# Performance work log

Measured on AMD Instinct MI355X. Metric: run time of the kernel, lower is better.

The kernel has to match this reference:

```python
import jax, jax.numpy as jnp
import numpy as np

B, T, H, POOL, MAX_ITER = 32, 1024, 128, 16, 4
D = 2 * H  # feature size of U rows


def _maxout(x, w, b, out_dim, pool):
    # x: [..., fin], w: [fin, out_dim*pool], b: [out_dim*pool]
    y = x @ w + b
    y = y.reshape(y.shape[:-1] + (out_dim, pool))
    return y.max(axis=-1)


def _hmn(U, us, ue, h, WDw, WDb, W1w, W1b, W2w, W2b, W3w, W3b):
    # U: [B,T,2H]; us, ue: [B,2H]; h: [B,H] -> scores [B,T]
    r = jnp.tanh(jnp.concatenate([h, us, ue], axis=-1) @ WDw + WDb)  # [B,H]
    rt = jnp.broadcast_to(r[:, None, :], (U.shape[0], U.shape[1], r.shape[-1]))
    m1 = _maxout(jnp.concatenate([U, rt], axis=-1), W1w, W1b, H, POOL)  # [B,T,H]
    m2 = _maxout(m1, W2w, W2b, H, POOL)                                  # [B,T,H]
    m3 = _maxout(jnp.concatenate([m1, m2], axis=-1), W3w, W3b, 1, POOL)  # [B,T,1]
    return m3[..., 0]  # [B,T]


def _lstm_cell(x, h, c, wih, whh, bih, bhh):
    gates = x @ wih.T + bih + h @ whh.T + bhh  # [B,4H]
    i, f, g, o = jnp.split(gates, 4, axis=-1)
    i, f, o = jax.nn.sigmoid(i), jax.nn.sigmoid(f), jax.nn.sigmoid(o)
    g = jnp.tanh(g)
    c2 = f * c + i * g
    h2 = o * jnp.tanh(c2)
    return h2, c2


def setup_inputs() -> dict:
    key = jax.random.key(0)
    ks = jax.random.split(key, 24)
    s = 0.05
    gn = lambda k, shape: (jax.random.normal(k, shape, jnp.float32) * s)
    inp = {"U": jax.random.normal(ks[0], (B, T, D), jnp.float32)}
    for tag, off in (("s", 1), ("e", 9)):
        inp[f"WD{tag}_w"] = gn(ks[off + 0], (5 * H, H))
        inp[f"WD{tag}_b"] = jnp.zeros((H,), jnp.float32)
        inp[f"W1{tag}_w"] = gn(ks[off + 1], (3 * H, H * POOL))
        inp[f"W1{tag}_b"] = jnp.zeros((H * POOL,), jnp.float32)
        inp[f"W2{tag}_w"] = gn(ks[off + 2], (H, H * POOL))
        inp[f"W2{tag}_b"] = jnp.zeros((H * POOL,), jnp.float32)
        inp[f"W3{tag}_w"] = gn(ks[off + 3], (2 * H, POOL))
        inp[f"W3{tag}_b"] = jnp.zeros((POOL,), jnp.float32)
    inp["lstm_wih"] = gn(ks[20], (4 * H, 4 * H))
    inp["lstm_whh"] = gn(ks[21], (4 * H, H))
    inp["lstm_bih"] = jnp.zeros((4 * H,), jnp.float32)
    inp["lstm_bhh"] = jnp.zeros((4 * H,), jnp.float32)
    return inp


def reference(U,
              WDs_w, WDs_b, W1s_w, W1s_b, W2s_w, W2s_b, W3s_w, W3s_b,
              WDe_w, WDe_b, W1e_w, W1e_b, W2e_w, W2e_b, W3e_w, W3e_b,
              lstm_wih, lstm_whh, lstm_bih, lstm_bhh):
    b = U.shape[0]
    bidx = jnp.arange(b)
    h = jnp.zeros((b, H), U.dtype)
    c = jnp.zeros((b, H), U.dtype)
    us, ue = U[:, 0, :], U[:, 1, :]
    entropies = []
    for _ in range(MAX_ITER):  # training-mode: run all iterations (no host-sync early stop)
        alpha_sc = _hmn(U, us, ue, h, WDs_w, WDs_b, W1s_w, W1s_b, W2s_w, W2s_b, W3s_w, W3s_b)
        alpha = jnp.argmax(alpha_sc, axis=1)           # [B]
        us = U[bidx, alpha, :]                          # data-dependent gather
        beta_sc = _hmn(U, us, ue, h, WDe_w, WDe_b, W1e_w, W1e_b, W2e_w, W2e_b, W3e_w, W3e_b)
        beta = jnp.argmax(beta_sc, axis=1)
        ue = U[bidx, beta, :]
        h, c = _lstm_cell(jnp.concatenate([us, ue], axis=1), h, c,
                          lstm_wih, lstm_whh, lstm_bih, lstm_bhh)
        entropies.append(jnp.stack([alpha_sc, beta_sc], axis=0))
    ent = jnp.stack(entropies, axis=0)  # [max_iter, 2, B, T]
    return alpha, beta, ent
```

## Files before the change

kernel.cpp:

```cpp
#include <hip/hip_runtime.h>
#include <math.h>

static constexpr int cB = 32;
static constexpr int cT = 1024;
static constexpr int cH = 128;
static constexpr int cD = 256;
static constexpr int cN = 2048;
static constexpr int cM = cB * cT;

typedef __attribute__((ext_vector_type(8))) short short8;
typedef __attribute__((ext_vector_type(4))) float f32x4;

__device__ __forceinline__ ushort f2bf(float x) {
    union { float f; unsigned u; } v; v.f = x;
    unsigned r = v.u + 0x7FFF + ((v.u >> 16) & 1);
    return (ushort)(r >> 16);
}
__device__ __forceinline__ float bf2f(ushort h) {
    union { float f; unsigned u; } v; v.u = ((unsigned)h) << 16;
    return v.f;
}

__device__ __forceinline__ void gload_lds16(const ushort* g, ushort* l) {
    __builtin_amdgcn_global_load_lds(
        (const __attribute__((address_space(1))) unsigned int*)(const void*)g,
        (__attribute__((address_space(3))) unsigned int*)(void*)l,
        16, 0, 0);
}

__global__ __launch_bounds__(256, 2)
void mfma_pool_m2(const ushort* __restrict__ Wth, const ushort* __restrict__ Wtl,
                  const ushort* __restrict__ Xh, const ushort* __restrict__ Xl,
                  const float* __restrict__ bias, float* __restrict__ out)
{
    constexpr int K = 128, S = 4;
    __shared__ __attribute__((aligned(16))) ushort sWh[128 * 128];
    __shared__ __attribute__((aligned(16))) ushort sWl[128 * 128];

    const int tid  = threadIdx.x;
    const int wave = tid >> 6;
    const int lane = tid & 63;
    const int l15  = lane & 15;
    const int lg   = lane >> 4;
    const int wr   = wave >> 1;
    const int wc   = wave & 1;

    const int wg  = blockIdx.x;
    const int lin = (wg & 7) * 128 + (wg >> 3);
    const int bx  = lin & 15;
    const int by  = lin >> 4;
    const int n0  = bx * 128;

    float ivv[4][4];
    #pragma unroll
    for (int rf = 0; rf < 4; ++rf)
        #pragma unroll
        for (int r = 0; r < 4; ++r)
            ivv[rf][r] = bias[n0 + wr * 64 + rf * 16 + lg * 4 + r];

    const int st_row_lo = lane >> 4;
    const int st_slot   = lane & 15;
    #pragma unroll
    for (int j = 0; j < 8; ++j) {
        int i   = wave * 8 + j;
        int row = i * 4 + st_row_lo;
        int ck  = st_slot ^ (row & 7);
        size_t goff = (size_t)(n0 + row) * K + ck * 8;
        gload_lds16(Wth + goff, sWh + i * 512);
        gload_lds16(Wtl + goff, sWl + i * 512);
    }
    __syncthreads();

    const int NP = 128;
    #pragma unroll
    for (int s = 0; s < S; ++s) {
        const int m0 = by * 512 + s * 128;

        short8 xh_[16], xl_[16];
        #pragma unroll
        for (int cf = 0; cf < 4; ++cf)
            #pragma unroll
            for (int ks = 0; ks < 4; ++ks) {
                size_t off = (size_t)(m0 + wc * 64 + cf * 16 + l15) * K
                           + ks * 32 + lg * 8;
                xh_[cf * 4 + ks] = *(const short8*)(Xh + off);
                xl_[cf * 4 + ks] = *(const short8*)(Xl + off);
            }

        f32x4 acc[4][4];
        #pragma unroll
        for (int rf = 0; rf < 4; ++rf)
            #pragma unroll
            for (int cf = 0; cf < 4; ++cf)
                acc[rf][cf] = (f32x4){0.f, 0.f, 0.f, 0.f};

        #pragma unroll
        for (int ks = 0; ks < 4; ++ks) {
            short8 w_h[4], w_l[4];
            #pragma unroll
            for (int rf = 0; rf < 4; ++rf) {
                int row  = wr * 64 + rf * 16 + l15;
                int ck2  = ks * 4 + lg;
                int adr  = row * 128 + ((ck2 ^ (row & 7)) * 8);
                w_h[rf] = *(const short8*)(sWh + adr);
                w_l[rf] = *(const short8*)(sWl + adr);
            }
            #pragma unroll
            for (int rf = 0; rf < 4; ++rf)
                #pragma unroll
                for (int cf = 0; cf < 4; ++cf) {
                    acc[rf][cf] = __builtin_amdgcn_mfma_f32_16x16x32_bf16(
                        w_h[rf], xh_[cf * 4 + ks], acc[rf][cf], 0, 0, 0);
                    acc[rf][cf] = __builtin_amdgcn_mfma_f32_16x16x32_bf16(
                        w_l[rf], xh_[cf * 4 + ks], acc[rf][cf], 0, 0, 0);
                    acc[rf][cf] = __builtin_amdgcn_mfma_f32_16x16x32_bf16(
                        w_h[rf], xl_[cf * 4 + ks], acc[rf][cf], 0, 0, 0);
                }
        }

        #pragma unroll
        for (int rf = 0; rf < 4; ++rf) {
            const int o2 = (n0 >> 4) + wr * 4 + rf;
            #pragma unroll
            for (int cf = 0; cf < 4; ++cf) {
                float v0 = acc[rf][cf][0] + ivv[rf][0];
                float v1 = acc[rf][cf][1] + ivv[rf][1];
                float v2 = acc[rf][cf][2] + ivv[rf][2];
                float v3 = acc[rf][cf][3] + ivv[rf][3];
                float mx = fmaxf(fmaxf(v0, v1), fmaxf(v2, v3));
                mx = fmaxf(mx, __shfl_xor(mx, 16));
                mx = fmaxf(mx, __shfl_xor(mx, 32));
                if (lane < 16) {
                    int m = m0 + wc * 64 + cf * 16 + lane;
                    out[(size_t)m * NP + o2] = mx;
                }
            }
        }
    }
}

template<int K, bool WRITE_HL>
__global__ __launch_bounds__(256, 2)
void mfma_pool_swp(const ushort* __restrict__ Wth, const ushort* __restrict__ Wtl,
                   const ushort* __restrict__ Xh, const ushort* __restrict__ Xl,
                   const float* __restrict__ initv, int init_bstride,
                   float* __restrict__ out, ushort* __restrict__ outh,
                   ushort* __restrict__ outl)
{
    constexpr int KH = K / 128;
    __shared__ __attribute__((aligned(16))) ushort sWh[128 * 128];
    __shared__ __attribute__((aligned(16))) ushort sWl[128 * 128];

    const int tid  = threadIdx.x;
    const int wave = tid >> 6;
    const int lane = tid & 63;
    const int l15  = lane & 15;
    const int lg   = lane >> 4;
    const int wr   = wave >> 1;
    const int wc   = wave & 1;

    const int wg  = blockIdx.x;
    const int lin = (wg & 7) * 512 + (wg >> 3);
    const int bx  = lin & 15;
    const int by  = lin >> 4;
    const int n0  = bx * 128;
    const int m0  = by * 128;
    const size_t ibase = (size_t)(m0 >> 10) * init_bstride;

    float ivv[4][4];
    #pragma unroll
    for (int rf = 0; rf < 4; ++rf)
        #pragma unroll
        for (int r = 0; r < 4; ++r)
            ivv[rf][r] = initv[ibase + n0 + wr * 64 + rf * 16 + lg * 4 + r];

    f32x4 acc[4][4];
    #pragma unroll
    for (int rf = 0; rf < 4; ++rf)
        #pragma unroll
        for (int cf = 0; cf < 4; ++cf)
            acc[rf][cf] = (f32x4){0.f, 0.f, 0.f, 0.f};

    const int st_row_lo = lane >> 4;
    const int st_slot   = lane & 15;

    #pragma unroll
    for (int kh = 0; kh < KH; ++kh) {
        const int kb = kh * 128;
        if (kh > 0) __syncthreads();

        #pragma unroll
        for (int j = 0; j < 8; ++j) {
            int i   = wave * 8 + j;
            int row = i * 4 + st_row_lo;
            int ck  = st_slot ^ (row & 7);
            size_t goff = (size_t)(n0 + row) * K + kb + ck * 8;
            gload_lds16(Wth + goff, sWh + i * 512);
            gload_lds16(Wtl + goff, sWl + i * 512);
        }
        short8 xh_[16], xl_[16];
        #pragma unroll
        for (int cf = 0; cf < 4; ++cf)
            #pragma unroll
            for (int ks = 0; ks < 4; ++ks) {
                size_t off = (size_t)(m0 + wc * 64 + cf * 16 + l15) * K
                           + kb + ks * 32 + lg * 8;
                xh_[cf * 4 + ks] = *(const short8*)(Xh + off);
                xl_[cf * 4 + ks] = *(const short8*)(Xl + off);
            }
        __syncthreads();

        #pragma unroll
        for (int ks = 0; ks < 4; ++ks) {
            short8 w_h[4], w_l[4];
            #pragma unroll
            for (int rf = 0; rf < 4; ++rf) {
                int row  = wr * 64 + rf * 16 + l15;
                int ck2  = ks * 4 + lg;
                int adr  = row * 128 + ((ck2 ^ (row & 7)) * 8);
                w_h[rf] = *(const short8*)(sWh + adr);
                w_l[rf] = *(const short8*)(sWl + adr);
            }
            #pragma unroll
            for (int rf = 0; rf < 4; ++rf)
                #pragma unroll
                for (int cf = 0; cf < 4; ++cf) {
                    acc[rf][cf] = __builtin_amdgcn_mfma_f32_16x16x32_bf16(
                        w_h[rf], xh_[cf * 4 + ks], acc[rf][cf], 0, 0, 0);
                    acc[rf][cf] = __builtin_amdgcn_mfma_f32_16x16x32_bf16(
                        w_l[rf], xh_[cf * 4 + ks], acc[rf][cf], 0, 0, 0);
                    acc[rf][cf] = __builtin_amdgcn_mfma_f32_16x16x32_bf16(
                        w_h[rf], xl_[cf * 4 + ks], acc[rf][cf], 0, 0, 0);
                }
        }
    }

    const int NP = 128;
    #pragma unroll
    for (int rf = 0; rf < 4; ++rf) {
        const int o2 = (n0 >> 4) + wr * 4 + rf;
        #pragma unroll
        for (int cf = 0; cf < 4; ++cf) {
            float v0 = acc[rf][cf][0] + ivv[rf][0];
            float v1 = acc[rf][cf][1] + ivv[rf][1];
            float v2 = acc[rf][cf][2] + ivv[rf][2];
            float v3 = acc[rf][cf][3] + ivv[rf][3];
            float mx = fmaxf(fmaxf(v0, v1), fmaxf(v2, v3));
            mx = fmaxf(mx, __shfl_xor(mx, 16));
            mx = fmaxf(mx, __shfl_xor(mx, 32));
            if (lane < 16) {
                int m = m0 + wc * 64 + cf * 16 + lane;
                size_t o = (size_t)m * NP + o2;
                out[o] = mx;
                if (WRITE_HL) {
                    ushort hb = f2bf(mx);
                    outh[o] = hb;
                    outl[o] = f2bf(mx - bf2f(hb));
                }
            }
        }
    }
}

__global__ void wsplit_kernel(const float* __restrict__ W, int K, int N,
                              ushort* __restrict__ th, ushort* __restrict__ tl)
{
    int idx = blockIdx.x * 256 + threadIdx.x;
    if (idx >= K * N) return;
    int k = idx / N, n = idx - k * N;
    float x = W[idx];
    ushort h = f2bf(x);
    th[(size_t)n * K + k] = h;
    tl[(size_t)n * K + k] = f2bf(x - bf2f(h));
}

__global__ void usplit_kernel(const float* __restrict__ U,
                              ushort* __restrict__ uh, ushort* __restrict__ ul)
{
    int idx = blockIdx.x * 256 + threadIdx.x;
    float x = U[idx];
    ushort h = f2bf(x);
    uh[idx] = h;
    ul[idx] = f2bf(x - bf2f(h));
}

__global__ void r_kernel(const float* __restrict__ h, const float* __restrict__ us,
                         const float* __restrict__ ue,
                         const float* __restrict__ WDw, const float* __restrict__ WDb,
                         float* __restrict__ r)
{
    int b = blockIdx.x;
    int j = threadIdx.x;
    __shared__ float x[640];
    x[j]       = h[b * cH + j];
    x[128 + j] = us[b * cD + j];
    x[256 + j] = us[b * cD + 128 + j];
    x[384 + j] = ue[b * cD + j];
    x[512 + j] = ue[b * cD + 128 + j];
    __syncthreads();
    float s = WDb[j];
    for (int k = 0; k < 640; ++k) s = fmaf(x[k], WDw[(size_t)k * cH + j], s);
    r[b * cH + j] = tanhf(s);
}

__global__ void rterm_kernel(const float* __restrict__ r, const float* __restrict__ W1r,
                             const float* __restrict__ W1b, float* __restrict__ rterm)
{
    int b = blockIdx.y;
    int n = blockIdx.x * 256 + threadIdx.x;
    __shared__ float rs[128];
    if (threadIdx.x < 128) rs[threadIdx.x] = r[b * cH + threadIdx.x];
    __syncthreads();
    float s = W1b[n];
    for (int k = 0; k < 128; ++k) s = fmaf(rs[k], W1r[(size_t)k * cN + n], s);
    rterm[(size_t)b * cN + n] = s;
}

__global__ __launch_bounds__(256)
void score_kernel(const float* __restrict__ m1, const float* __restrict__ m2,
                  const float* __restrict__ W3w, const float* __restrict__ W3b,
                  float* __restrict__ ent)
{
    __shared__ float xs[16][257];
    __shared__ float wsh[256 * 16];
    int tid = threadIdx.x;
    int m0 = blockIdx.x * 16;
    #pragma unroll
    for (int q = 0; q < 16; ++q) wsh[tid + q * 256] = W3w[tid + q * 256];
    #pragma unroll
    for (int q = 0; q < 8; ++q) {
        int f = tid + q * 256;
        int rl = f >> 7, col = f & 127;
        xs[rl][col]       = m1[(size_t)(m0 + rl) * cH + col];
        xs[rl][128 + col] = m2[(size_t)(m0 + rl) * cH + col];
    }
    __syncthreads();
    int rl = tid >> 4, p = tid & 15;
    float s = W3b[p];
    for (int k = 0; k < 256; ++k) s = fmaf(xs[rl][k], wsh[k * 16 + p], s);
    #pragma unroll
    for (int off = 8; off; off >>= 1) s = fmaxf(s, __shfl_xor(s, off));
    if (p == 0) ent[m0 + rl] = s;
}

__global__ void argmax_kernel(const float* __restrict__ sc, const float* __restrict__ U,
                              float* __restrict__ uvec, float* __restrict__ outidx)
{
    int b = blockIdx.x;
    int tid = threadIdx.x;
    float bv = -3.4e38f;
    int bi = 0x7fffffff;
    for (int t = tid; t < cT; t += 256) {
        float v = sc[b * cT + t];
        if (v > bv || (v == bv && t < bi)) { bv = v; bi = t; }
    }
    __shared__ float vs[256];
    __shared__ int   is[256];
    vs[tid] = bv; is[tid] = bi;
    __syncthreads();
    for (int s = 128; s > 0; s >>= 1) {
        if (tid < s) {
            if (vs[tid + s] > vs[tid] ||
                (vs[tid + s] == vs[tid] && is[tid + s] < is[tid])) {
                vs[tid] = vs[tid + s];
                is[tid] = is[tid + s];
            }
        }
        __syncthreads();
    }
    int best = is[0];
    if (tid == 0) outidx[b] = (float)best;
    uvec[b * cD + tid % cD] = U[((size_t)b * cT + best) * cD + (tid % cD)];
}

__global__ void lstm_kernel(const float* __restrict__ us, const float* __restrict__ ue,
                            float* __restrict__ h, float* __restrict__ c,
                            const float* __restrict__ wih, const float* __restrict__ whh,
                            const float* __restrict__ bih, const float* __restrict__ bhh)
{
    int b = blockIdx.x;
    int j = threadIdx.x;
    __shared__ float x[512];
    __shared__ float hh[128];
    x[j]       = us[b * cD + j];
    x[128 + j] = us[b * cD + 128 + j];
    x[256 + j] = ue[b * cD + j];
    x[384 + j] = ue[b * cD + 128 + j];
    hh[j] = h[b * cH + j];
    __syncthreads();
    float g4[4];
    #pragma unroll
    for (int gi = 0; gi < 4; ++gi) {
        int row = gi * 128 + j;
        float s = bih[row] + bhh[row];
        const float* wr = wih + (size_t)row * 512;
        for (int k = 0; k < 512; ++k) s = fmaf(x[k], wr[k], s);
        const float* wr2 = whh + (size_t)row * 128;
        for (int k = 0; k < 128; ++k) s = fmaf(hh[k], wr2[k], s);
        g4[gi] = s;
    }
    float i_ = 1.f / (1.f + expf(-g4[0]));
    float f_ = 1.f / (1.f + expf(-g4[1]));
    float g_ = tanhf(g4[2]);
    float o_ = 1.f / (1.f + expf(-g4[3]));
    float c2 = f_ * c[b * cH + j] + i_ * g_;
    float h2 = o_ * tanhf(c2);
    c[b * cH + j] = c2;
    h[b * cH + j] = h2;
}

__global__ void init_kernel(const float* __restrict__ U, float* __restrict__ us,
                            float* __restrict__ ue, float* __restrict__ h,
                            float* __restrict__ c)
{
    int i = blockIdx.x * 256 + threadIdx.x;
    if (i < cB * cD) {
        int b = i >> 8, d = i & 255;
        us[i] = U[((size_t)b * cT + 0) * cD + d];
        ue[i] = U[((size_t)b * cT + 1) * cD + d];
    }
    if (i < cB * cH) { h[i] = 0.f; c[i] = 0.f; }
}

extern "C" void kernel_launch(void* const* d_in, const int* in_sizes, int n_in,
                              void* d_out, int out_size, void* d_ws, size_t ws_size,
                              hipStream_t stream)
{
    const float* U = (const float*)d_in[0];
    const float* WD_w[2] = {(const float*)d_in[1], (const float*)d_in[9]};
    const float* WD_b[2] = {(const float*)d_in[2], (const float*)d_in[10]};
    const float* W1_w[2] = {(const float*)d_in[3], (const float*)d_in[11]};
    const float* W1_b[2] = {(const float*)d_in[4], (const float*)d_in[12]};
    const float* W2_w[2] = {(const float*)d_in[5], (const float*)d_in[13]};
    const float* W2_b[2] = {(const float*)d_in[6], (const float*)d_in[14]};
    const float* W3_w[2] = {(const float*)d_in[7], (const float*)d_in[15]};
    const float* W3_b[2] = {(const float*)d_in[8], (const float*)d_in[16]};
    const float* wih = (const float*)d_in[17];
    const float* whh = (const float*)d_in[18];
    const float* bih = (const float*)d_in[19];
    const float* bhh = (const float*)d_in[20];

    float* ws = (float*)d_ws;
    float* m1 = ws;
    float* m2 = m1 + (size_t)cM * cH;
    float* us = m2 + (size_t)cM * cH;
    float* ue = us + cB * cD;
    float* h  = ue + cB * cD;
    float* c  = h + cB * cH;
    float* r  = c + cB * cH;
    float* rterm = r + cB * cH;
    float* cur = rterm + (size_t)cB * cN;

    ushort* m1h = (ushort*)cur;                   cur += (size_t)cM * cH / 2;
    ushort* m1l = (ushort*)cur;                   cur += (size_t)cM * cH / 2;
    ushort* Uh  = (ushort*)cur;                   cur += (size_t)cM * cD / 2;
    ushort* Ul  = (ushort*)cur;                   cur += (size_t)cM * cD / 2;
    ushort* W1th[2], *W1tl[2], *W2th[2], *W2tl[2];
    for (int sd = 0; sd < 2; ++sd) {
        W1th[sd] = (ushort*)cur; cur += (size_t)cN * cD / 2;
        W1tl[sd] = (ushort*)cur; cur += (size_t)cN * cD / 2;
        W2th[sd] = (ushort*)cur; cur += (size_t)cN * cH / 2;
        W2tl[sd] = (ushort*)cur; cur += (size_t)cN * cH / 2;
    }

    float* outf = (float*)d_out;

    init_kernel<<<32, 256, 0, stream>>>(U, us, ue, h, c);
    usplit_kernel<<<(cM * cD) / 256, 256, 0, stream>>>(U, Uh, Ul);
    for (int sd = 0; sd < 2; ++sd) {
        wsplit_kernel<<<(cD * cN) / 256, 256, 0, stream>>>(
            W1_w[sd], cD, cN, W1th[sd], W1tl[sd]);
        wsplit_kernel<<<(cH * cN) / 256, 256, 0, stream>>>(
            W2_w[sd], cH, cN, W2th[sd], W2tl[sd]);
    }

    const int ggrid = (cN / 128) * (cM / 128);
    for (int it = 0; it < 4; ++it) {
        for (int sd = 0; sd < 2; ++sd) {
            r_kernel<<<32, 128, 0, stream>>>(h, us, ue, WD_w[sd], WD_b[sd], r);
            rterm_kernel<<<dim3(8, 32), 256, 0, stream>>>(
                r, W1_w[sd] + (size_t)256 * cN, W1_b[sd], rterm);
            mfma_pool_swp<256, true><<<ggrid, 256, 0, stream>>>(
                W1th[sd], W1tl[sd], Uh, Ul, rterm, cN, m1, m1h, m1l);
            mfma_pool_m2<<<1024, 256, 0, stream>>>(
                W2th[sd], W2tl[sd], m1h, m1l, W2_b[sd], m2);
            float* ent = outf + 64 + (size_t)(it * 2 + sd) * cB * cT;
            score_kernel<<<2048, 256, 0, stream>>>(m1, m2, W3_w[sd], W3_b[sd], ent);
            argmax_kernel<<<32, 256, 0, stream>>>(ent, U, sd ? ue : us,
                                                  outf + (sd ? 32 : 0));
        }
        lstm_kernel<<<32, 128, 0, stream>>>(us, ue, h, c, wih, whh, bih, bhh);
    }
}
```

Measured before the change: 2.802 ms.

## Double-buffer W1 LDS tiles in m1 GEMM with async prefetch of next K-chunk

Replaces the m1 maxout GEMM kernel with a version that splits K=256 into four 64-wide chunks and double-buffers the weight tiles in LDS. The global-to-LDS loads for the next chunk are issued before computing the current one, with explicit vmcnt waits and barriers. The aim is to hide weight-load latency behind MFMA work instead of stalling on each 128-wide half. In exchange it adds more barrier points, and the X fragments are now loaded per chunk without being overlapped.

```diff
diff --git a/kernel.cpp b/kernel.cpp
--- a/kernel.cpp
+++ b/kernel.cpp
@@ -26,6 +26,144 @@
         (const __attribute__((address_space(1))) unsigned int*)(const void*)g,
         (__attribute__((address_space(3))) unsigned int*)(void*)l,
         16, 0, 0);
+}
+
+__global__ __launch_bounds__(256, 2)
+void m1_pipe_kernel(const ushort* __restrict__ Wth, const ushort* __restrict__ Wtl,
+                    const ushort* __restrict__ Xh, const ushort* __restrict__ Xl,
+                    const float* __restrict__ rterm,
+                    float* __restrict__ out, ushort* __restrict__ outh,
+                    ushort* __restrict__ outl)
+{
+    constexpr int K = 256;
+    __shared__ __attribute__((aligned(16))) ushort sWh[2 * 8192];
+    __shared__ __attribute__((aligned(16))) ushort sWl[2 * 8192];
+
+    const int tid  = threadIdx.x;
+    const int wave = tid >> 6;
+    const int lane = tid & 63;
+    const int l15  = lane & 15;
+    const int lg   = lane >> 4;
+    const int wn   = wave >> 1;
+    const int wm   = wave & 1;
+
+    const int wg  = blockIdx.x;
+    const int lin = (wg & 7) * 512 + (wg >> 3);
+    const int bx  = lin & 15;
+    const int by  = lin >> 4;
+    const int n0  = bx * 128;
+    const int m0  = by * 128;
+    const size_t ibase = (size_t)(m0 >> 10) * cN;
+
+    float ivv[4][4];
+    #pragma unroll
+    for (int rf = 0; rf < 4; ++rf)
+        #pragma unroll
+        for (int r = 0; r < 4; ++r)
+            ivv[rf][r] = rterm[ibase + n0 + wn * 64 + rf * 16 + lg * 4 + r];
+
+    f32x4 acc[4][4];
+    #pragma unroll
+    for (int rf = 0; rf < 4; ++rf)
+        #pragma unroll
+        for (int cf = 0; cf < 4; ++cf)
+            acc[rf][cf] = (f32x4){0.f, 0.f, 0.f, 0.f};
+
+    const int st_r = lane >> 3;
+    const int st_s = lane & 7;
+
+    #pragma unroll
+    for (int j = 0; j < 4; ++j) {
+        int i   = wave * 4 + j;
+        int row = i * 8 + st_r;
+        int ck  = st_s ^ (row & 7);
+        size_t goff = (size_t)(n0 + row) * K + ck * 8;
+        gload_lds16(Wth + goff, sWh + i * 512);
+        gload_lds16(Wtl + goff, sWl + i * 512);
+    }
+
+    #pragma unroll
+    for (int t = 0; t < 4; ++t) {
+        const int cb = (t & 1) * 8192;
+        if (t > 0) __builtin_amdgcn_s_barrier();
+        if (t < 3) {
+            const int nb = ((t + 1) & 1) * 8192;
+            const int kt = (t + 1) * 64;
+            #pragma unroll
+            for (int j = 0; j < 4; ++j) {
+                int i   = wave * 4 + j;
+                int row = i * 8 + st_r;
+                int ck  = st_s ^ (row & 7);
+                size_t goff = (size_t)(n0 + row) * K + kt + ck * 8;
+                gload_lds16(Wth + goff, sWh + nb + i * 512);
+                gload_lds16(Wtl + goff, sWl + nb + i * 512);
+            }
+            asm volatile("s_waitcnt vmcnt(8)" ::: "memory");
+        } else {
+            asm volatile("s_waitcnt vmcnt(0)" ::: "memory");
+        }
+        __builtin_amdgcn_s_barrier();
+        __builtin_amdgcn_sched_barrier(0);
+
+        short8 xh_[8], xl_[8];
+        #pragma unroll
+        for (int cf = 0; cf < 4; ++cf)
+            #pragma unroll
+            for (int ks = 0; ks < 2; ++ks) {
+                size_t off = (size_t)(m0 + wm * 64 + cf * 16 + l15) * K
+                           + t * 64 + ks * 32 + lg * 8;
+                xh_[cf * 2 + ks] = *(const short8*)(Xh + off);
+                xl_[cf * 2 + ks] = *(const short8*)(Xl + off);
+            }
+
+        #pragma unroll
+        for (int ks = 0; ks < 2; ++ks) {
+            short8 w_h[4], w_l[4];
+            #pragma unroll
+            for (int rf = 0; rf < 4; ++rf) {
+                int row  = wn * 64 + rf * 16 + l15;
+                int ck2  = ks * 4 + lg;
+                int adr  = cb + row * 64 + ((ck2 ^ (row & 7)) * 8);
+                w_h[rf] = *(const short8*)(sWh + adr);
+                w_l[rf] = *(const short8*)(sWl + adr);
+            }
+            #pragma unroll
+            for (int rf = 0; rf < 4; ++rf)
+                #pragma unroll
+                for (int cf = 0; cf < 4; ++cf) {
+                    acc[rf][cf] = __builtin_amdgcn_mfma_f32_16x16x32_bf16(
+                        w_h[rf], xh_[cf * 2 + ks], acc[rf][cf], 0, 0, 0);
+                    acc[rf][cf] = __builtin_amdgcn_mfma_f32_16x16x32_bf16(
+                        w_l[rf], xh_[cf * 2 + ks], acc[rf][cf], 0, 0, 0);
+                    acc[rf][cf] = __builtin_amdgcn_mfma_f32_16x16x32_bf16(
+                        w_h[rf], xl_[cf * 2 + ks], acc[rf][cf], 0, 0, 0);
+                }
+        }
+    }
+
+    const int NP = 128;
+    #pragma unroll
+    for (int rf = 0; rf < 4; ++rf) {
+        const int o2 = (n0 >> 4) + wn * 4 + rf;
+        #pragma unroll
+        for (int cf = 0; cf < 4; ++cf) {
+            float v0 = acc[rf][cf][0] + ivv[rf][0];
+            float v1 = acc[rf][cf][1] + ivv[rf][1];
+            float v2 = acc[rf][cf][2] + ivv[rf][2];
+            float v3 = acc[rf][cf][3] + ivv[rf][3];
+            float mx = fmaxf(fmaxf(v0, v1), fmaxf(v2, v3));
+            mx = fmaxf(mx, __shfl_xor(mx, 16));
+            mx = fmaxf(mx, __shfl_xor(mx, 32));
+            if (lane < 16) {
+                int m = m0 + wm * 64 + cf * 16 + lane;
+                size_t o = (size_t)m * NP + o2;
+                out[o] = mx;
+                ushort hb = f2bf(mx);
+                outh[o] = hb;
+                outl[o] = f2bf(mx - bf2f(hb));
+            }
+        }
+    }
 }
 
 __global__ __launch_bounds__(256, 2)
@@ -133,129 +271,6 @@
                 if (lane < 16) {
                     int m = m0 + wc * 64 + cf * 16 + lane;
                     out[(size_t)m * NP + o2] = mx;
-                }
-            }
-        }
-    }
-}
-
-template<int K, bool WRITE_HL>
-__global__ __launch_bounds__(256, 2)
-void mfma_pool_swp(const ushort* __restrict__ Wth, const ushort* __restrict__ Wtl,
-                   const ushort* __restrict__ Xh, const ushort* __restrict__ Xl,
-                   const float* __restrict__ initv, int init_bstride,
-                   float* __restrict__ out, ushort* __restrict__ outh,
-                   ushort* __restrict__ outl)
-{
-    constexpr int KH = K / 128;
-    __shared__ __attribute__((aligned(16))) ushort sWh[128 * 128];
-    __shared__ __attribute__((aligned(16))) ushort sWl[128 * 128];
-
-    const int tid  = threadIdx.x;
-    const int wave = tid >> 6;
-    const int lane = tid & 63;
-    const int l15  = lane & 15;
-    const int lg   = lane >> 4;
-    const int wr   = wave >> 1;
-    const int wc   = wave & 1;
-
-    const int wg  = blockIdx.x;
-    const int lin = (wg & 7) * 512 + (wg >> 3);
-    const int bx  = lin & 15;
-    const int by  = lin >> 4;
-    const int n0  = bx * 128;
-    const int m0  = by * 128;
-    const size_t ibase = (size_t)(m0 >> 10) * init_bstride;
-
-    float ivv[4][4];
-    #pragma unroll
-    for (int rf = 0; rf < 4; ++rf)
-        #pragma unroll
-        for (int r = 0; r < 4; ++r)
-            ivv[rf][r] = initv[ibase + n0 + wr * 64 + rf * 16 + lg * 4 + r];
-
-    f32x4 acc[4][4];
-    #pragma unroll
-    for (int rf = 0; rf < 4; ++rf)
-        #pragma unroll
-        for (int cf = 0; cf < 4; ++cf)
-            acc[rf][cf] = (f32x4){0.f, 0.f, 0.f, 0.f};
-
-    const int st_row_lo = lane >> 4;
-    const int st_slot   = lane & 15;
-
-    #pragma unroll
-    for (int kh = 0; kh < KH; ++kh) {
-        const int kb = kh * 128;
-        if (kh > 0) __syncthreads();
-
-        #pragma unroll
-        for (int j = 0; j < 8; ++j) {
-            int i   = wave * 8 + j;
-            int row = i * 4 + st_row_lo;
-            int ck  = st_slot ^ (row & 7);
-            size_t goff = (size_t)(n0 + row) * K + kb + ck * 8;
-            gload_lds16(Wth + goff, sWh + i * 512);
-            gload_lds16(Wtl + goff, sWl + i * 512);
-        }
-        short8 xh_[16], xl_[16];
-        #pragma unroll
-        for (int cf = 0; cf < 4; ++cf)
-            #pragma unroll
-            for (int ks = 0; ks < 4; ++ks) {
-                size_t off = (size_t)(m0 + wc * 64 + cf * 16 + l15) * K
-                           + kb + ks * 32 + lg * 8;
-                xh_[cf * 4 + ks] = *(const short8*)(Xh + off);
-                xl_[cf * 4 + ks] = *(const short8*)(Xl + off);
-            }
-        __syncthreads();
-
-        #pragma unroll
-        for (int ks = 0; ks < 4; ++ks) {
-            short8 w_h[4], w_l[4];
-            #pragma unroll
-            for (int rf = 0; rf < 4; ++rf) {
-                int row  = wr * 64 + rf * 16 + l15;
-                int ck2  = ks * 4 + lg;
-                int adr  = row * 128 + ((ck2 ^ (row & 7)) * 8);
-                w_h[rf] = *(const short8*)(sWh + adr);
-                w_l[rf] = *(const short8*)(sWl + adr);
-            }
-            #pragma unroll
-            for (int rf = 0; rf < 4; ++rf)
-                #pragma unroll
-                for (int cf = 0; cf < 4; ++cf) {
-                    acc[rf][cf] = __builtin_amdgcn_mfma_f32_16x16x32_bf16(
-                        w_h[rf], xh_[cf * 4 + ks], acc[rf][cf], 0, 0, 0);
-                    acc[rf][cf] = __builtin_amdgcn_mfma_f32_16x16x32_bf16(
-                        w_l[rf], xh_[cf * 4 + ks], acc[rf][cf], 0, 0, 0);
-                    acc[rf][cf] = __builtin_amdgcn_mfma_f32_16x16x32_bf16(
-                        w_h[rf], xl_[cf * 4 + ks], acc[rf][cf], 0, 0, 0);
-                }
-        }
-    }
-
-    const int NP = 128;
-    #pragma unroll
-    for (int rf = 0; rf < 4; ++rf) {
-        const int o2 = (n0 >> 4) + wr * 4 + rf;
-        #pragma unroll
-        for (int cf = 0; cf < 4; ++cf) {
-            float v0 = acc[rf][cf][0] + ivv[rf][0];
-            float v1 = acc[rf][cf][1] + ivv[rf][1];
-            float v2 = acc[rf][cf][2] + ivv[rf][2];
-            float v3 = acc[rf][cf][3] + ivv[rf][3];
-            float mx = fmaxf(fmaxf(v0, v1), fmaxf(v2, v3));
-            mx = fmaxf(mx, __shfl_xor(mx, 16));
-            mx = fmaxf(mx, __shfl_xor(mx, 32));
-            if (lane < 16) {
-                int m = m0 + wc * 64 + cf * 16 + lane;
-                size_t o = (size_t)m * NP + o2;
-                out[o] = mx;
-                if (WRITE_HL) {
-                    ushort hb = f2bf(mx);
-                    outh[o] = hb;
-                    outl[o] = f2bf(mx - bf2f(hb));
                 }
             }
         }
@@ -480,8 +495,8 @@
             r_kernel<<<32, 128, 0, stream>>>(h, us, ue, WD_w[sd], WD_b[sd], r);
             rterm_kernel<<<dim3(8, 32), 256, 0, stream>>>(
                 r, W1_w[sd] + (size_t)256 * cN, W1_b[sd], rterm);
-            mfma_pool_swp<256, true><<<ggrid, 256, 0, stream>>>(
-                W1th[sd], W1tl[sd], Uh, Ul, rterm, cN, m1, m1h, m1l);
+            m1_pipe_kernel<<<ggrid, 256, 0, stream>>>(
+                W1th[sd], W1tl[sd], Uh, Ul, rterm, m1, m1h, m1l);
             mfma_pool_m2<<<1024, 256, 0, stream>>>(
                 W2th[sd], W2tl[sd], m1h, m1l, W2_b[sd], m2);
             float* ent = outf + 64 + (size_t)(it * 2 + sd) * cB * cT;
```

Measured after the change: 2.788 ms. No clear change (-0.5%).
